# Optimization experiments

Measured on AMD Instinct MI355X. Metric: run time of the kernel, lower is better.

The kernel has to match this reference:

```python
import jax, jax.numpy as jnp
import numpy as np

N_NODES = 100000
N_EDGES = 1600000
IN = 128
HID = 128
OUT_CLS = 40
EPS = 1e-12


def setup_inputs() -> dict:
    key = jax.random.key(0)
    ks = jax.random.split(key, 12)
    feat = jax.random.normal(ks[0], (N_NODES, IN), dtype=jnp.float32)
    edge_index = jax.random.randint(ks[1], (2, N_EDGES), 0, N_NODES, dtype=jnp.int64)

    def xavier(k, shape):
        fan_out, fan_in = shape
        lim = float(np.sqrt(6.0 / (fan_in + fan_out)))
        return jax.random.uniform(k, shape, jnp.float32, -lim, lim)

    return {
        "feat": feat,
        "edge_index": edge_index,
        "Wl1": xavier(ks[2], (HID, IN)),  "bl1": jnp.zeros((HID,), jnp.float32), "Wr1": xavier(ks[3], (HID, IN)),
        "Wl2": xavier(ks[4], (HID, HID)), "bl2": jnp.zeros((HID,), jnp.float32), "Wr2": xavier(ks[5], (HID, HID)),
        "Wl3": xavier(ks[6], (HID, HID)), "bl3": jnp.zeros((HID,), jnp.float32), "Wr3": xavier(ks[7], (HID, HID)),
        "Wfc": xavier(ks[8], (OUT_CLS, HID)), "bfc": jnp.zeros((OUT_CLS,), jnp.float32),
    }


def sage_conv(x, src, dst, Wl, bl, Wr):
    # mean-aggregate neighbor messages x[src] into dst nodes (PyG aggr='mean')
    agg = jax.ops.segment_sum(x[src], dst, num_segments=N_NODES)        # [N, d]
    cnt = jax.ops.segment_sum(jnp.ones((src.shape[0],), x.dtype), dst,
                              num_segments=N_NODES)                      # [N]
    agg = agg / jnp.maximum(cnt, 1.0)[:, None]
    out = agg @ Wl.T + bl + x @ Wr.T                                     # lin_l(agg) + lin_r(x)
    # F.normalize(p=2, dim=-1, eps=1e-12)
    norm = jnp.linalg.norm(out, axis=-1, keepdims=True)
    return out / jnp.maximum(norm, EPS)


def reference(feat, edge_index, Wl1, bl1, Wr1, Wl2, bl2, Wr2, Wl3, bl3, Wr3, Wfc, bfc):
    src, dst = edge_index[0], edge_index[1]
    h = jax.nn.relu(sage_conv(feat, src, dst, Wl1, bl1, Wr1))
    h = jax.nn.relu(sage_conv(h, src, dst, Wl2, bl2, Wr2))
    h = sage_conv(h, src, dst, Wl3, bl3, Wr3)
    logits = h @ Wfc.T + bfc
    return jax.nn.softmax(logits, axis=-1)
```

## Files before the change

kernel.cpp:

```cpp
#include <hip/hip_runtime.h>
#include <cstdint>

#define N_NODES 100000
#define N_EDGES 1600000
#define F 128
#define OUT_CLS 40
#define LW 13
#define LBM (LW * 32)
#define BSHIFT 10
#define NBUCK 98
#define TILE 2048

using f32x16 = __attribute__((ext_vector_type(16))) float;
using bf16x8 = __attribute__((ext_vector_type(8))) short;
using f16x2 = __attribute__((ext_vector_type(2))) _Float16;

__device__ __forceinline__ int edge_val(const int* eb, int is64, long idx) {
  return is64 ? eb[2 * idx] : eb[idx];
}

__global__ void k_detect(const unsigned int* eb, int* flag) {
  if (threadIdx.x == 0 && blockIdx.x == 0) {
    int is64 = 1;
#pragma unroll
    for (int i = 1; i < 16; i += 2) is64 &= (eb[i] == 0u);
    flag[0] = is64;
  }
}

#define CH_E 16
__global__ __launch_bounds__(256) void k_chist(const int* __restrict__ eb, const int* __restrict__ flag,
                                               int* __restrict__ bhist) {
  __shared__ int lh[NBUCK];
  int t = threadIdx.x;
  if (t < NBUCK) lh[t] = 0;
  __syncthreads();
  int is64 = flag[0];
  long base = (long)blockIdx.x * (256 * CH_E);
#pragma unroll
  for (int i = 0; i < CH_E; ++i) {
    long e = base + (long)i * 256 + t;
    if (e < N_EDGES) {
      int d = edge_val(eb, is64, (long)N_EDGES + e);
      atomicAdd(&lh[d >> BSHIFT], 1);
    }
  }
  __syncthreads();
  if (t < NBUCK && lh[t]) atomicAdd(&bhist[t], lh[t]);
}

__global__ __launch_bounds__(128) void k_bscan(const int* __restrict__ bhist, int* __restrict__ boff,
                                               int* __restrict__ bkt_cursor, int* __restrict__ off) {
  __shared__ int sh[128];
  int t = threadIdx.x;
  int v = (t < NBUCK) ? bhist[t] : 0;
  sh[t] = v;
  __syncthreads();
  for (int d = 1; d < 128; d <<= 1) {
    int u = (t >= d) ? sh[t - d] : 0;
    __syncthreads();
    sh[t] += u;
    __syncthreads();
  }
  int incl = sh[t];
  if (t < NBUCK) {
    boff[t] = incl - v;
    bkt_cursor[t] = incl - v;
  }
  if (t == NBUCK - 1) boff[NBUCK] = incl;
  if (t == 0) off[N_NODES] = N_EDGES;
}

__global__ __launch_bounds__(256) void k_bscatter(const int* __restrict__ eb, const int* __restrict__ flag,
                                                  int* __restrict__ bkt_cursor, uint2* __restrict__ ebuf) {
  __shared__ int lhist[128];
  __shared__ int lbase[128];
  __shared__ int gbase[NBUCK];
  __shared__ int lcnt[NBUCK];
  __shared__ uint2 buf[TILE];
  __shared__ int slotpos[TILE];
  int t = threadIdx.x;
  long e0 = (long)blockIdx.x * TILE;
  int is64 = flag[0];
  if (t < 128) lhist[t] = 0;
  __syncthreads();
#pragma unroll
  for (int i = 0; i < TILE / 256; ++i) {
    long e = e0 + t + i * 256;
    if (e < N_EDGES) {
      int d = edge_val(eb, is64, (long)N_EDGES + e);
      atomicAdd(&lhist[d >> BSHIFT], 1);
    }
  }
  __syncthreads();
  if (t < 128) lbase[t] = lhist[t];
  __syncthreads();
  for (int d = 1; d < 128; d <<= 1) {
    int v = (t >= d && t < 128) ? lbase[t - d] : 0;
    __syncthreads();
    if (t < 128) lbase[t] += v;
    __syncthreads();
  }
  if (t < NBUCK) {
    gbase[t] = atomicAdd(&bkt_cursor[t], lhist[t]);
    lcnt[t] = 0;
  }
  __syncthreads();
#pragma unroll
  for (int i = 0; i < TILE / 256; ++i) {
    long e = e0 + t + i * 256;
    if (e < N_EDGES) {
      int d = edge_val(eb, is64, (long)N_EDGES + e);
      int s = edge_val(eb, is64, e);
      int b = d >> BSHIFT;
      int n = atomicAdd(&lcnt[b], 1);
      int slot = lbase[b] - lhist[b] + n;
      buf[slot] = make_uint2((unsigned)s, (unsigned)d);
      slotpos[slot] = gbase[b] + n;
    }
  }
  __syncthreads();
  int tile_n = (int)min((long)TILE, (long)N_EDGES - e0);
  for (int i = t; i < tile_n; i += 256) {
    ebuf[slotpos[i]] = buf[i];
  }
}

__global__ __launch_bounds__(1024) void k_fsort(const uint2* __restrict__ ebuf, const int* __restrict__ boff,
                                                int* __restrict__ off, int* __restrict__ srcs) {
  __shared__ int hist[1024];
  __shared__ int cur[1024];
  __shared__ int wsum[16];
  int b = blockIdx.x;
  int t = threadIdx.x;
  int p0 = boff[b], p1 = boff[b + 1];
  hist[t] = 0;
  __syncthreads();
  for (int p = p0 + t; p < p1; p += 1024) {
    int d = (int)ebuf[p].y & 1023;
    atomicAdd(&hist[d], 1);
  }
  __syncthreads();
  int h = hist[t];
  int v = h;
#pragma unroll
  for (int o = 1; o < 64; o <<= 1) {
    int u = __shfl_up(v, o);
    if ((t & 63) >= o) v += u;
  }
  if ((t & 63) == 63) wsum[t >> 6] = v;
  __syncthreads();
  if (t < 64) {
    int w = (t < 16) ? wsum[t] : 0;
#pragma unroll
    for (int o = 1; o < 16; o <<= 1) {
      int u = __shfl_up(w, o);
      if (t >= o) w += u;
    }
    if (t < 16) wsum[t] = w;
  }
  __syncthreads();
  int base = (t >> 6) ? wsum[(t >> 6) - 1] : 0;
  int gpos = p0 + base + v - h;
  int node = (b << BSHIFT) + t;
  if (node < N_NODES) off[node] = gpos;
  cur[t] = gpos;
  __syncthreads();
  for (int p = p0 + t; p < p1; p += 1024) {
    uint2 sd = ebuf[p];
    int pos = atomicAdd(&cur[(int)sd.y & 1023], 1);
    srcs[pos] = (int)sd.x;
  }
}

__global__ __launch_bounds__(256) void k_tohalf(const float* __restrict__ in, _Float16* __restrict__ o) {
  int i = blockIdx.x * 256 + threadIdx.x;
  if (i >= N_NODES * F / 8) return;
  float4 a = reinterpret_cast<const float4*>(in)[2 * i];
  float4 b = reinterpret_cast<const float4*>(in)[2 * i + 1];
  union {
    _Float16 h[8];
    uint4 u;
  } r;
  r.h[0] = (_Float16)a.x; r.h[1] = (_Float16)a.y; r.h[2] = (_Float16)a.z; r.h[3] = (_Float16)a.w;
  r.h[4] = (_Float16)b.x; r.h[5] = (_Float16)b.y; r.h[6] = (_Float16)b.z; r.h[7] = (_Float16)b.w;
  reinterpret_cast<uint4*>(o)[i] = r.u;
}

__global__ __launch_bounds__(256) void k_aggregate(const _Float16* __restrict__ x, const int* __restrict__ off,
                                                   const int* __restrict__ srcs, float* __restrict__ agg) {
  int n = blockIdx.x * 4 + (threadIdx.x >> 6);
  if (n >= N_NODES) return;
  int l = threadIdx.x & 63;
  int p0 = off[n], p1 = off[n + 1];
  int deg = p1 - p0;
  float sx = 0.f, sy = 0.f;

  for (int base = 0; base < deg; base += 64) {
    int rem = deg - base;
    int cnt = (rem < 64) ? rem : 64;
    int my = (l < cnt) ? srcs[p0 + base + l] : 0;
    int j = 0;
    for (; j + 7 < cnt; j += 8) {
      int s[8];
#pragma unroll
      for (int k = 0; k < 8; ++k) s[k] = __builtin_amdgcn_readlane(my, j + k);
      f16x2 v[8];
#pragma unroll
      for (int k = 0; k < 8; ++k)
        v[k] = *reinterpret_cast<const f16x2*>(x + (size_t)(unsigned)s[k] * F + 2 * l);
#pragma unroll
      for (int k = 0; k < 8; ++k) {
        sx += (float)v[k][0];
        sy += (float)v[k][1];
      }
    }
    for (; j + 3 < cnt; j += 4) {
      int s[4];
#pragma unroll
      for (int k = 0; k < 4; ++k) s[k] = __builtin_amdgcn_readlane(my, j + k);
      f16x2 v[4];
#pragma unroll
      for (int k = 0; k < 4; ++k)
        v[k] = *reinterpret_cast<const f16x2*>(x + (size_t)(unsigned)s[k] * F + 2 * l);
#pragma unroll
      for (int k = 0; k < 4; ++k) {
        sx += (float)v[k][0];
        sy += (float)v[k][1];
      }
    }
    for (; j < cnt; ++j) {
      int s = __builtin_amdgcn_readlane(my, j);
      f16x2 v = *reinterpret_cast<const f16x2*>(x + (size_t)(unsigned)s * F + 2 * l);
      sx += (float)v[0];
      sy += (float)v[1];
    }
  }

  float inv = 1.0f / (float)max(deg, 1);
  float2 r;
  r.x = sx * inv;
  r.y = sy * inv;
  *reinterpret_cast<float2*>(agg + (size_t)n * F + 2 * l) = r;
}

__device__ __forceinline__ void split_pack(const float4& a, const float4& b, bf16x8& hi, bf16x8& lo) {
  float f[8] = {a.x, a.y, a.z, a.w, b.x, b.y, b.z, b.w};
#pragma unroll
  for (int i = 0; i < 8; ++i) {
    union { float f; unsigned u; } u0;
    u0.f = f[i];
    hi[i] = (short)(u0.u >> 16);
    union { unsigned u; float f; } uh;
    uh.u = u0.u & 0xFFFF0000u;
    union { float f; unsigned u; } ur;
    ur.f = f[i] - uh.f;
    lo[i] = (short)(ur.u >> 16);
  }
}

__global__ __launch_bounds__(256) void k_wsplit(const float* __restrict__ Wl1, const float* __restrict__ Wr1,
                                                const float* __restrict__ Wl2, const float* __restrict__ Wr2,
                                                const float* __restrict__ Wl3, const float* __restrict__ Wr3,
                                                unsigned short* __restrict__ wsp) {
  int e = blockIdx.x * 256 + threadIdx.x;
  if (e >= 3 * 16384) return;
  int L = e >> 14, off = e & 16383;
  const float* wl = (L == 0) ? Wl1 : (L == 1) ? Wl2 : Wl3;
  const float* wr = (L == 0) ? Wr1 : (L == 1) ? Wr2 : Wr3;
  unsigned short* base = wsp + (size_t)L * 4 * 16384;
  {
    union { float f; unsigned u; } u0;
    u0.f = wl[off];
    union { unsigned u; float f; } uh;
    uh.u = u0.u & 0xFFFF0000u;
    union { float f; unsigned u; } ur;
    ur.f = u0.f - uh.f;
    base[off] = (unsigned short)(u0.u >> 16);
    base[16384 + off] = (unsigned short)(ur.u >> 16);
  }
  {
    union { float f; unsigned u; } u0;
    u0.f = wr[off];
    union { unsigned u; float f; } uh;
    uh.u = u0.u & 0xFFFF0000u;
    union { float f; unsigned u; } ur;
    ur.f = u0.f - uh.f;
    base[2 * 16384 + off] = (unsigned short)(u0.u >> 16);
    base[3 * 16384 + off] = (unsigned short)(ur.u >> 16);
  }
}

__global__ __launch_bounds__(832, 1) void k_linear(const float* __restrict__ agg, const float* __restrict__ x,
                                                   const unsigned short* __restrict__ wsp,
                                                   const float* __restrict__ bl, float* out,
                                                   _Float16* __restrict__ out16, int relu) {
  __shared__ unsigned short wlds[4][128][136];
  int tid = threadIdx.x;

  for (int c = tid; c < 4 * 2048; c += 832) {
    int m = c >> 11, rem = c & 2047;
    int j = rem >> 4, kc = (rem & 15) * 8;
    uint4 v = *reinterpret_cast<const uint4*>(wsp + (size_t)m * 16384 + j * 128 + kc);
    *reinterpret_cast<uint4*>(&wlds[m][j][kc]) = v;
  }
  __syncthreads();

  int wid = tid >> 6, lane = tid & 63;
  int l31 = lane & 31, lhi = lane >> 5;
  long rb = (long)blockIdx.x * LBM + (long)wid * 32;
  if (rb >= N_NODES) return;

  int r0 = (int)min(rb + l31, (long)N_NODES - 1);
  const float* a0p = agg + (size_t)r0 * F + lhi * 8;
  const float* x0p = x + (size_t)r0 * F + lhi * 8;

  f32x16 acc[4];
#pragma unroll
  for (int ct = 0; ct < 4; ++ct) acc[ct] = (f32x16)0.f;

  float4 ap = *reinterpret_cast<const float4*>(a0p);
  float4 aq = *reinterpret_cast<const float4*>(a0p + 4);
  float4 xp = *reinterpret_cast<const float4*>(x0p);
  float4 xq = *reinterpret_cast<const float4*>(x0p + 4);

#pragma unroll
  for (int ks = 0; ks < 8; ++ks) {
    float4 ap_n, aq_n, xp_n, xq_n;
    if (ks < 7) {
      const float* an = a0p + (ks + 1) * 16;
      const float* xn = x0p + (ks + 1) * 16;
      ap_n = *reinterpret_cast<const float4*>(an);
      aq_n = *reinterpret_cast<const float4*>(an + 4);
      xp_n = *reinterpret_cast<const float4*>(xn);
      xq_n = *reinterpret_cast<const float4*>(xn + 4);
    }
    int k0 = ks * 16 + lhi * 8;
    bf16x8 aH0, aL0, xH0, xL0;
    split_pack(ap, aq, aH0, aL0);
    split_pack(xp, xq, xH0, xL0);
#pragma unroll
    for (int ct = 0; ct < 4; ++ct) {
      int j = ct * 32 + l31;
      bf16x8 BlH = *reinterpret_cast<const bf16x8*>(&wlds[0][j][k0]);
      bf16x8 BlL = *reinterpret_cast<const bf16x8*>(&wlds[1][j][k0]);
      bf16x8 BrH = *reinterpret_cast<const bf16x8*>(&wlds[2][j][k0]);
      bf16x8 BrL = *reinterpret_cast<const bf16x8*>(&wlds[3][j][k0]);
      acc[ct] = __builtin_amdgcn_mfma_f32_32x32x16_bf16(aH0, BlH, acc[ct], 0, 0, 0);
      acc[ct] = __builtin_amdgcn_mfma_f32_32x32x16_bf16(aL0, BlH, acc[ct], 0, 0, 0);
      acc[ct] = __builtin_amdgcn_mfma_f32_32x32x16_bf16(aH0, BlL, acc[ct], 0, 0, 0);
      acc[ct] = __builtin_amdgcn_mfma_f32_32x32x16_bf16(xH0, BrH, acc[ct], 0, 0, 0);
      acc[ct] = __builtin_amdgcn_mfma_f32_32x32x16_bf16(xL0, BrH, acc[ct], 0, 0, 0);
      acc[ct] = __builtin_amdgcn_mfma_f32_32x32x16_bf16(xH0, BrL, acc[ct], 0, 0, 0);
    }
    ap = ap_n;
    aq = aq_n;
    xp = xp_n;
    xq = xq_n;
  }

#pragma unroll
  for (int ct = 0; ct < 4; ++ct) {
    float b = bl[ct * 32 + l31];
#pragma unroll
    for (int i = 0; i < 16; ++i) acc[ct][i] += b;
  }
#pragma unroll
  for (int i = 0; i < 16; ++i) {
    float ss = acc[0][i] * acc[0][i] + acc[1][i] * acc[1][i] +
               acc[2][i] * acc[2][i] + acc[3][i] * acc[3][i];
#pragma unroll
    for (int o = 1; o < 32; o <<= 1) ss += __shfl_xor(ss, o);
    float inv = 1.0f / fmaxf(sqrtf(ss), 1e-12f);
    long grow = rb + (i & 3) + 8 * (i >> 2) + 4 * lhi;
    if (grow < N_NODES) {
      long base = grow * F + l31;
#pragma unroll
      for (int ct = 0; ct < 4; ++ct) {
        float v = acc[ct][i] * inv;
        if (relu) v = fmaxf(v, 0.f);
        out[base + ct * 32] = v;
        if (out16) out16[base + ct * 32] = (_Float16)v;
      }
    }
  }
}

#define FCP 132
__global__ __launch_bounds__(256) void k_fc_softmax(const float* __restrict__ h, const float* __restrict__ Wfc,
                                                    const float* __restrict__ bfc, float* __restrict__ out) {
  __shared__ float w_s[OUT_CLS][FCP];
  __shared__ float h_s[32][FCP];
  int tid = threadIdx.x;
  int nb = blockIdx.x * 32;

  for (int i = tid; i < OUT_CLS * (F / 4); i += 256) {
    int r = i >> 5, c = (i & 31) * 4;
    *reinterpret_cast<float4*>(&w_s[r][c]) = *reinterpret_cast<const float4*>(Wfc + (size_t)r * F + c);
  }
  for (int i = tid; i < 32 * (F / 4); i += 256) {
    int r = i >> 5, c = (i & 31) * 4;
    *reinterpret_cast<float4*>(&h_s[r][c]) = *reinterpret_cast<const float4*>(h + (size_t)(nb + r) * F + c);
  }
  __syncthreads();

  int r = tid >> 3, sub = tid & 7;
  float acc[5];
#pragma unroll
  for (int c = 0; c < 5; ++c) acc[c] = bfc[sub * 5 + c];

  for (int k4 = 0; k4 < F / 4; ++k4) {
    float4 hv = *reinterpret_cast<const float4*>(&h_s[r][k4 * 4]);
#pragma unroll
    for (int c = 0; c < 5; ++c) {
      float4 wv = *reinterpret_cast<const float4*>(&w_s[sub * 5 + c][k4 * 4]);
      acc[c] += hv.x * wv.x + hv.y * wv.y + hv.z * wv.z + hv.w * wv.w;
    }
  }

  float m = acc[0];
#pragma unroll
  for (int c = 1; c < 5; ++c) m = fmaxf(m, acc[c]);
#pragma unroll
  for (int o = 4; o > 0; o >>= 1) m = fmaxf(m, __shfl_xor(m, o));
  float e[5], s = 0.f;
#pragma unroll
  for (int c = 0; c < 5; ++c) {
    e[c] = expf(acc[c] - m);
    s += e[c];
  }
#pragma unroll
  for (int o = 4; o > 0; o >>= 1) s += __shfl_xor(s, o);
  float inv = 1.0f / s;
#pragma unroll
  for (int c = 0; c < 5; ++c) out[(size_t)(nb + r) * OUT_CLS + sub * 5 + c] = e[c] * inv;
}

extern "C" void kernel_launch(void* const* d_in, const int* in_sizes, int n_in, void* d_out, int out_size,
                              void* d_ws, size_t ws_size, hipStream_t stream) {
  const float* feat = (const float*)d_in[0];
  const int* eb = (const int*)d_in[1];
  const float* Wl1 = (const float*)d_in[2];
  const float* bl1 = (const float*)d_in[3];
  const float* Wr1 = (const float*)d_in[4];
  const float* Wl2 = (const float*)d_in[5];
  const float* bl2 = (const float*)d_in[6];
  const float* Wr2 = (const float*)d_in[7];
  const float* Wl3 = (const float*)d_in[8];
  const float* bl3 = (const float*)d_in[9];
  const float* Wr3 = (const float*)d_in[10];
  const float* Wfc = (const float*)d_in[11];
  const float* bfc = (const float*)d_in[12];
  float* out = (float*)d_out;

  char* w = (char*)d_ws;
  auto alloc = [&](size_t bytes) {
    char* p = w;
    w += (bytes + 255) & ~(size_t)255;
    return p;
  };
  int* flag = (int*)alloc(4);
  int* bhist = (int*)alloc((size_t)NBUCK * 4);
  int* boff = (int*)alloc((size_t)(NBUCK + 1) * 4);
  int* off = (int*)alloc((size_t)(N_NODES + 1) * 4);
  int* srcs = (int*)alloc((size_t)N_EDGES * 4);
  int* bkt_cursor = (int*)alloc((size_t)NBUCK * 4);
  unsigned short* wsp = (unsigned short*)alloc((size_t)3 * 4 * 16384 * 2);
  float* bufA = (float*)alloc((size_t)N_NODES * F * 4);
  float* bufB = (float*)alloc((size_t)N_NODES * F * 4);
  _Float16* h16X = (_Float16*)alloc((size_t)N_NODES * F * 2);
  _Float16* h16A = (_Float16*)alloc((size_t)N_NODES * F * 2);
  uint2* ebuf = (uint2*)bufB;
  (void)ws_size;
  (void)in_sizes;
  (void)n_in;
  (void)out_size;

  hipMemsetAsync(bhist, 0, (size_t)NBUCK * 4, stream);
  k_detect<<<1, 64, 0, stream>>>((const unsigned int*)eb, flag);
  k_chist<<<(N_EDGES + 256 * CH_E - 1) / (256 * CH_E), 256, 0, stream>>>(eb, flag, bhist);
  k_bscan<<<1, 128, 0, stream>>>(bhist, boff, bkt_cursor, off);
  k_bscatter<<<(N_EDGES + TILE - 1) / TILE, 256, 0, stream>>>(eb, flag, bkt_cursor, ebuf);
  k_fsort<<<NBUCK, 1024, 0, stream>>>(ebuf, boff, off, srcs);
  k_wsplit<<<192, 256, 0, stream>>>(Wl1, Wr1, Wl2, Wr2, Wl3, Wr3, wsp);
  k_tohalf<<<(N_NODES * F / 8 + 255) / 256, 256, 0, stream>>>(feat, h16X);

  const int nag = (N_NODES + 3) / 4;
  const int nlin = (N_NODES + LBM - 1) / LBM;
  const int nfc = N_NODES / 32;

  k_aggregate<<<nag, 256, 0, stream>>>(h16X, off, srcs, bufA);
  k_linear<<<nlin, 832, 0, stream>>>(bufA, feat, wsp + 0 * 4 * 16384, bl1, bufA, h16A, 1);
  k_aggregate<<<nag, 256, 0, stream>>>(h16A, off, srcs, bufB);
  k_linear<<<nlin, 832, 0, stream>>>(bufB, bufA, wsp + 1 * 4 * 16384, bl2, bufB, h16X, 1);
  k_aggregate<<<nag, 256, 0, stream>>>(h16X, off, srcs, bufA);
  k_linear<<<nlin, 832, 0, stream>>>(bufA, bufB, wsp + 2 * 4 * 16384, bl3, bufA, ((_Float16*)0), 0);
  k_fc_softmax<<<nfc, 256, 0, stream>>>(bufA, Wfc, bfc, out);
}
```

Baseline: 418.2 us.

## Gather two neighbor rows per wave with 8-byte loads, two nodes per wave

The aggregation kernel now splits each wavefront into two halves. Each half reads a different neighbor row using 8-byte fp16x4 loads, and the halves are combined with a cross-half shuffle. Each wave also handles two nodes, and both nodes' first source-index batches are loaded up front, which halves the grid size. The aim is more memory-level parallelism and fewer load instructions per edge in the gather, at the cost of a shuffle reduction and half-idle lanes on odd-degree tails and the final store.

```diff
diff --git a/kernel.cpp b/kernel.cpp
--- a/kernel.cpp
+++ b/kernel.cpp
@@ -14,6 +14,7 @@
 using f32x16 = __attribute__((ext_vector_type(16))) float;
 using bf16x8 = __attribute__((ext_vector_type(8))) short;
 using f16x2 = __attribute__((ext_vector_type(2))) _Float16;
+using f16x4 = __attribute__((ext_vector_type(4))) _Float16;
 
 __device__ __forceinline__ int edge_val(const int* eb, int is64, long idx) {
   return is64 ? eb[2 * idx] : eb[idx];
@@ -187,61 +188,111 @@
   reinterpret_cast<uint4*>(o)[i] = r.u;
 }
 
-__global__ __launch_bounds__(256) void k_aggregate(const _Float16* __restrict__ x, const int* __restrict__ off,
-                                                   const int* __restrict__ srcs, float* __restrict__ agg) {
-  int n = blockIdx.x * 4 + (threadIdx.x >> 6);
-  if (n >= N_NODES) return;
-  int l = threadIdx.x & 63;
-  int p0 = off[n], p1 = off[n + 1];
-  int deg = p1 - p0;
-  float sx = 0.f, sy = 0.f;
-
+__device__ __forceinline__ void gather_node(const _Float16* __restrict__ x, const int* __restrict__ srcs,
+                                            int p0, int deg, int my0, int l, int half, int c4,
+                                            float& s0, float& s1, float& s2, float& s3) {
+  s0 = s1 = s2 = s3 = 0.f;
   for (int base = 0; base < deg; base += 64) {
     int rem = deg - base;
     int cnt = (rem < 64) ? rem : 64;
-    int my = (l < cnt) ? srcs[p0 + base + l] : 0;
+    int my = base ? ((l < cnt) ? srcs[p0 + base + l] : 0) : my0;
     int j = 0;
-    for (; j + 7 < cnt; j += 8) {
-      int s[8];
-#pragma unroll
-      for (int k = 0; k < 8; ++k) s[k] = __builtin_amdgcn_readlane(my, j + k);
-      f16x2 v[8];
-#pragma unroll
-      for (int k = 0; k < 8; ++k)
-        v[k] = *reinterpret_cast<const f16x2*>(x + (size_t)(unsigned)s[k] * F + 2 * l);
+    for (; j + 15 < cnt; j += 16) {
+      f16x4 v[8];
 #pragma unroll
       for (int k = 0; k < 8; ++k) {
-        sx += (float)v[k][0];
-        sy += (float)v[k][1];
+        int sE = __builtin_amdgcn_readlane(my, j + 2 * k);
+        int sO = __builtin_amdgcn_readlane(my, j + 2 * k + 1);
+        int s = half ? sO : sE;
+        v[k] = *reinterpret_cast<const f16x4*>(x + (size_t)(unsigned)s * F + c4);
       }
-    }
-    for (; j + 3 < cnt; j += 4) {
-      int s[4];
-#pragma unroll
-      for (int k = 0; k < 4; ++k) s[k] = __builtin_amdgcn_readlane(my, j + k);
-      f16x2 v[4];
-#pragma unroll
-      for (int k = 0; k < 4; ++k)
-        v[k] = *reinterpret_cast<const f16x2*>(x + (size_t)(unsigned)s[k] * F + 2 * l);
-#pragma unroll
-      for (int k = 0; k < 4; ++k) {
-        sx += (float)v[k][0];
-        sy += (float)v[k][1];
+#pragma unroll
+      for (int k = 0; k < 8; ++k) {
+        s0 += (float)v[k][0];
+        s1 += (float)v[k][1];
+        s2 += (float)v[k][2];
+        s3 += (float)v[k][3];
       }
     }
-    for (; j < cnt; ++j) {
+    for (; j + 1 < cnt; j += 2) {
+      int sE = __builtin_amdgcn_readlane(my, j);
+      int sO = __builtin_amdgcn_readlane(my, j + 1);
+      int s = half ? sO : sE;
+      f16x4 v = *reinterpret_cast<const f16x4*>(x + (size_t)(unsigned)s * F + c4);
+      s0 += (float)v[0];
+      s1 += (float)v[1];
+      s2 += (float)v[2];
+      s3 += (float)v[3];
+    }
+    if (j < cnt) {
       int s = __builtin_amdgcn_readlane(my, j);
-      f16x2 v = *reinterpret_cast<const f16x2*>(x + (size_t)(unsigned)s * F + 2 * l);
-      sx += (float)v[0];
-      sy += (float)v[1];
-    }
-  }
-
-  float inv = 1.0f / (float)max(deg, 1);
-  float2 r;
-  r.x = sx * inv;
-  r.y = sy * inv;
-  *reinterpret_cast<float2*>(agg + (size_t)n * F + 2 * l) = r;
+      f16x4 v = *reinterpret_cast<const f16x4*>(x + (size_t)(unsigned)s * F + c4);
+      if (!half) {
+        s0 += (float)v[0];
+        s1 += (float)v[1];
+        s2 += (float)v[2];
+        s3 += (float)v[3];
+      }
+    }
+  }
+}
+
+__global__ __launch_bounds__(256) void k_aggregate(const _Float16* __restrict__ x, const int* __restrict__ off,
+                                                   const int* __restrict__ srcs, float* __restrict__ agg) {
+  int w = threadIdx.x >> 6;
+  int l = threadIdx.x & 63;
+  int half = l >> 5;
+  int c4 = (l & 31) * 4;
+  int nA = blockIdx.x * 8 + w;
+  if (nA >= N_NODES) return;
+  int nB = nA + 4;
+  bool hasB = (nB < N_NODES);
+
+  int pA0 = off[nA], pA1 = off[nA + 1];
+  int pB0 = 0, pB1 = 0;
+  if (hasB) {
+    pB0 = off[nB];
+    pB1 = off[nB + 1];
+  }
+  int degA = pA1 - pA0, degB = pB1 - pB0;
+  int cA = (degA < 64) ? degA : 64;
+  int cB = (degB < 64) ? degB : 64;
+  int myA = (l < cA) ? srcs[pA0 + l] : 0;
+  int myB = (hasB && l < cB) ? srcs[pB0 + l] : 0;
+
+  float a0, a1, a2, a3;
+  gather_node(x, srcs, pA0, degA, myA, l, half, c4, a0, a1, a2, a3);
+  a0 += __shfl_xor(a0, 32);
+  a1 += __shfl_xor(a1, 32);
+  a2 += __shfl_xor(a2, 32);
+  a3 += __shfl_xor(a3, 32);
+  float invA = 1.0f / (float)((degA > 1) ? degA : 1);
+  if (half == 0) {
+    float4 r;
+    r.x = a0 * invA;
+    r.y = a1 * invA;
+    r.z = a2 * invA;
+    r.w = a3 * invA;
+    *reinterpret_cast<float4*>(agg + (size_t)nA * F + c4) = r;
+  }
+
+  if (hasB) {
+    float b0, b1, b2, b3;
+    gather_node(x, srcs, pB0, degB, myB, l, half, c4, b0, b1, b2, b3);
+    b0 += __shfl_xor(b0, 32);
+    b1 += __shfl_xor(b1, 32);
+    b2 += __shfl_xor(b2, 32);
+    b3 += __shfl_xor(b3, 32);
+    float invB = 1.0f / (float)((degB > 1) ? degB : 1);
+    if (half == 0) {
+      float4 r;
+      r.x = b0 * invB;
+      r.y = b1 * invB;
+      r.z = b2 * invB;
+      r.w = b3 * invB;
+      *reinterpret_cast<float4*>(agg + (size_t)nB * F + c4) = r;
+    }
+  }
 }
 
 __device__ __forceinline__ void split_pack(const float4& a, const float4& b, bf16x8& hi, bf16x8& lo) {
@@ -485,7 +536,7 @@
   k_wsplit<<<192, 256, 0, stream>>>(Wl1, Wr1, Wl2, Wr2, Wl3, Wr3, wsp);
   k_tohalf<<<(N_NODES * F / 8 + 255) / 256, 256, 0, stream>>>(feat, h16X);
 
-  const int nag = (N_NODES + 3) / 4;
+  const int nag = (N_NODES + 7) / 8;
   const int nlin = (N_NODES + LBM - 1) / LBM;
   const int nfc = N_NODES / 32;
 
```

After: 417.7 us. No clear change (-0.1%).

## Slice fp16 features into 16-column planes so the gather works on one slice at a time

Applied to the files above, without the earlier changes.

Stores the fp16 node features as eight column slices of 16 values each. Each slice is stored contiguously across all nodes, giving a 3.2 MB working set per slice that fits in cache. The aggregate kernel now assigns each block one slice, and every wavefront handles 8 nodes with 8 edges gathered in parallel (8 lanes per edge), then reduces with shuffles. The aim is better cache hit rates on random neighbour gathers. The cost is extra index redundancy: offsets and source lists are read eight times, once per slice. The fp16 writes in the linear kernel become scattered.

```diff
diff --git a/kernel.cpp b/kernel.cpp
--- a/kernel.cpp
+++ b/kernel.cpp
@@ -174,74 +174,69 @@
 }
 
 __global__ __launch_bounds__(256) void k_tohalf(const float* __restrict__ in, _Float16* __restrict__ o) {
-  int i = blockIdx.x * 256 + threadIdx.x;
-  if (i >= N_NODES * F / 8) return;
-  float4 a = reinterpret_cast<const float4*>(in)[2 * i];
-  float4 b = reinterpret_cast<const float4*>(in)[2 * i + 1];
+  int c = blockIdx.x * 256 + threadIdx.x;
+  if (c >= N_NODES * F / 8) return;
+  int h = c & 1;
+  int n = (c >> 1) % N_NODES;
+  int sl = (c >> 1) / N_NODES;
+  const float* src = in + (size_t)n * F + sl * 16 + h * 8;
+  float4 a = *reinterpret_cast<const float4*>(src);
+  float4 b = *reinterpret_cast<const float4*>(src + 4);
   union {
-    _Float16 h[8];
+    _Float16 hh[8];
     uint4 u;
   } r;
-  r.h[0] = (_Float16)a.x; r.h[1] = (_Float16)a.y; r.h[2] = (_Float16)a.z; r.h[3] = (_Float16)a.w;
-  r.h[4] = (_Float16)b.x; r.h[5] = (_Float16)b.y; r.h[6] = (_Float16)b.z; r.h[7] = (_Float16)b.w;
-  reinterpret_cast<uint4*>(o)[i] = r.u;
-}
-
-__global__ __launch_bounds__(256) void k_aggregate(const _Float16* __restrict__ x, const int* __restrict__ off,
+  r.hh[0] = (_Float16)a.x; r.hh[1] = (_Float16)a.y; r.hh[2] = (_Float16)a.z; r.hh[3] = (_Float16)a.w;
+  r.hh[4] = (_Float16)b.x; r.hh[5] = (_Float16)b.y; r.hh[6] = (_Float16)b.z; r.hh[7] = (_Float16)b.w;
+  *reinterpret_cast<uint4*>(o + (size_t)c * 8) = r.u;
+}
+
+__global__ __launch_bounds__(256) void k_aggregate(const _Float16* __restrict__ xs,
+                                                   const int* __restrict__ off,
                                                    const int* __restrict__ srcs, float* __restrict__ agg) {
-  int n = blockIdx.x * 4 + (threadIdx.x >> 6);
-  if (n >= N_NODES) return;
+  int sl = blockIdx.x & 7;
+  int chunk = blockIdx.x >> 3;
+  int w = threadIdx.x >> 6;
   int l = threadIdx.x & 63;
-  int p0 = off[n], p1 = off[n + 1];
-  int deg = p1 - p0;
-  float sx = 0.f, sy = 0.f;
-
-  for (int base = 0; base < deg; base += 64) {
-    int rem = deg - base;
-    int cnt = (rem < 64) ? rem : 64;
-    int my = (l < cnt) ? srcs[p0 + base + l] : 0;
-    int j = 0;
-    for (; j + 7 < cnt; j += 8) {
-      int s[8];
-#pragma unroll
-      for (int k = 0; k < 8; ++k) s[k] = __builtin_amdgcn_readlane(my, j + k);
-      f16x2 v[8];
-#pragma unroll
-      for (int k = 0; k < 8; ++k)
-        v[k] = *reinterpret_cast<const f16x2*>(x + (size_t)(unsigned)s[k] * F + 2 * l);
-#pragma unroll
-      for (int k = 0; k < 8; ++k) {
-        sx += (float)v[k][0];
-        sy += (float)v[k][1];
+  int g = l >> 3;
+  int fo = (l & 7) * 2;
+  const _Float16* xb = xs + (size_t)sl * N_NODES * 16;
+  int n0 = chunk * 32 + w * 8;
+  for (int ni = 0; ni < 8; ++ni) {
+    int n = n0 + ni;
+    if (n >= N_NODES) return;
+    int p0 = __builtin_nontemporal_load(off + n);
+    int p1 = __builtin_nontemporal_load(off + n + 1);
+    int deg = p1 - p0;
+    float s0 = 0.f, s1 = 0.f;
+    for (int base = 0; base < deg; base += 64) {
+      int rem = deg - base;
+      int cnt = (rem < 64) ? rem : 64;
+      int my = (l < cnt) ? __builtin_nontemporal_load(srcs + p0 + base + l) : 0;
+      for (int j = 0; j < cnt; j += 8) {
+        int idx = j + g;
+        int s = __shfl(my, idx);
+        f16x2 v = *reinterpret_cast<const f16x2*>(xb + (size_t)(unsigned)s * 16 + fo);
+        if (idx < cnt) {
+          s0 += (float)v[0];
+          s1 += (float)v[1];
+        }
       }
     }
-    for (; j + 3 < cnt; j += 4) {
-      int s[4];
-#pragma unroll
-      for (int k = 0; k < 4; ++k) s[k] = __builtin_amdgcn_readlane(my, j + k);
-      f16x2 v[4];
-#pragma unroll
-      for (int k = 0; k < 4; ++k)
-        v[k] = *reinterpret_cast<const f16x2*>(x + (size_t)(unsigned)s[k] * F + 2 * l);
-#pragma unroll
-      for (int k = 0; k < 4; ++k) {
-        sx += (float)v[k][0];
-        sy += (float)v[k][1];
-      }
-    }
-    for (; j < cnt; ++j) {
-      int s = __builtin_amdgcn_readlane(my, j);
-      f16x2 v = *reinterpret_cast<const f16x2*>(x + (size_t)(unsigned)s * F + 2 * l);
-      sx += (float)v[0];
-      sy += (float)v[1];
-    }
-  }
-
-  float inv = 1.0f / (float)max(deg, 1);
-  float2 r;
-  r.x = sx * inv;
-  r.y = sy * inv;
-  *reinterpret_cast<float2*>(agg + (size_t)n * F + 2 * l) = r;
+    s0 += __shfl_xor(s0, 8);
+    s1 += __shfl_xor(s1, 8);
+    s0 += __shfl_xor(s0, 16);
+    s1 += __shfl_xor(s1, 16);
+    s0 += __shfl_xor(s0, 32);
+    s1 += __shfl_xor(s1, 32);
+    float inv = 1.0f / (float)((deg > 1) ? deg : 1);
+    if (l < 8) {
+      float2 r;
+      r.x = s0 * inv;
+      r.y = s1 * inv;
+      *reinterpret_cast<float2*>(agg + (size_t)n * F + sl * 16 + l * 2) = r;
+    }
+  }
 }
 
 __device__ __forceinline__ void split_pack(const float4& a, const float4& b, bf16x8& hi, bf16x8& lo) {
@@ -380,7 +375,10 @@
         float v = acc[ct][i] * inv;
         if (relu) v = fmaxf(v, 0.f);
         out[base + ct * 32] = v;
-        if (out16) out16[base + ct * 32] = (_Float16)v;
+        if (out16) {
+          int f = ct * 32 + l31;
+          out16[((size_t)(f >> 4) * N_NODES + grow) * 16 + (f & 15)] = (_Float16)v;
+        }
       }
     }
   }
@@ -463,7 +461,7 @@
   int* bhist = (int*)alloc((size_t)NBUCK * 4);
   int* boff = (int*)alloc((size_t)(NBUCK + 1) * 4);
   int* off = (int*)alloc((size_t)(N_NODES + 1) * 4);
-  int* srcs = (int*)alloc((size_t)N_EDGES * 4);
+  int* srcs = (int*)alloc((size_t)N_EDGES * 4 + 256);
   int* bkt_cursor = (int*)alloc((size_t)NBUCK * 4);
   unsigned short* wsp = (unsigned short*)alloc((size_t)3 * 4 * 16384 * 2);
   float* bufA = (float*)alloc((size_t)N_NODES * F * 4);
@@ -485,7 +483,7 @@
   k_wsplit<<<192, 256, 0, stream>>>(Wl1, Wr1, Wl2, Wr2, Wl3, Wr3, wsp);
   k_tohalf<<<(N_NODES * F / 8 + 255) / 256, 256, 0, stream>>>(feat, h16X);
 
-  const int nag = (N_NODES + 3) / 4;
+  const int nag = 8 * ((N_NODES + 31) / 32);
   const int nlin = (N_NODES + LBM - 1) / LBM;
   const int nfc = N_NODES / 32;
 
```

Result: slower. 983.9 us (+135.3%).
